# Kernel tuning notes

Measured on AMD Instinct MI355X. Metric: run time of the kernel, lower is better.

Reference implementation:

```python
import jax, jax.numpy as jnp
import numpy as np

B = 32768
K = 4096  # num_embeddings
D = 512   # embedding_dim
COMMITMENT_COST = 0.25


def setup_inputs() -> dict:
    key = jax.random.key(0)
    k1, k2 = jax.random.split(key)
    inputs = jax.random.normal(k1, (B, D), dtype=jnp.float32)
    # nn.Embedding weight init: uniform(-1/K, 1/K)
    codebook = jax.random.uniform(k2, (K, D), dtype=jnp.float32,
                                  minval=-1.0 / K, maxval=1.0 / K)
    return {"inputs": inputs, "codebook": codebook}


def reference(inputs, codebook):
    distances = (jnp.sum(inputs ** 2, axis=1, keepdims=True)
                 + jnp.sum(codebook ** 2, axis=1)
                 - 2.0 * jnp.matmul(inputs, codebook.T))
    encoding_indices = jnp.argmin(distances, axis=1)  # [B]
    # one-hot encodings are part of the module's returned dict
    encodings = jax.nn.one_hot(encoding_indices, K, dtype=inputs.dtype)  # [B, K]
    # quantized = encodings @ codebook == direct gather (same math)
    quantized = codebook[encoding_indices]  # [B, D]

    sg = jax.lax.stop_gradient
    e_latent_loss = jnp.mean((sg(quantized) - inputs) ** 2)
    q_latent_loss = jnp.mean((quantized - sg(inputs)) ** 2)
    loss = q_latent_loss + COMMITMENT_COST * e_latent_loss

    # straight-through estimator
    quantized_st = inputs + sg(quantized - inputs)

    avg_probs = jnp.mean(encodings, axis=0)  # [K]
    perplexity = jnp.exp(-jnp.sum(avg_probs * jnp.log(avg_probs + 1e-10)))

    return quantized_st, encoding_indices, loss, perplexity, encodings
```

## Files before the change

### kernel.cpp

```cpp
#include <hip/hip_runtime.h>
#include <hip/hip_bf16.h>


typedef __attribute__((ext_vector_type(8))) short bf16x8;
typedef __attribute__((ext_vector_type(4))) float f32x4;

#define BB 32768
#define KK 4096
#define DD 512

#define IDX_OFF  (BB*DD)
#define LOSS_OFF (IDX_OFF + BB)
#define PERP_OFF (LOSS_OFF + 1)
#define ENC_OFF  (PERP_OFF + 1)

#define WSB_XSQ  0
#define WSB_ESQ  131072
#define WSB_IDX  147456
#define WSB_HIST 278528
#define WSB_LOSS 294912
#define WSB_EBF3 294928
#define WSB_XBF  4489232
#define WSB_PART 38043664

#define MARG 2.5e-4f
#define NCAND 16

static __device__ __forceinline__ unsigned short f2bf(float f) {
    __hip_bfloat16 h = __float2bfloat16(f);
    return *reinterpret_cast<unsigned short*>(&h);
}

static __device__ __forceinline__ unsigned int packscore(float s, int col) {
    unsigned int u = __float_as_uint(s);
    u ^= (u & 0x80000000u) ? 0xFFFFFFFFu : 0x80000000u;
    return (u & 0xFFFFF000u) | (unsigned int)col;
}
static __device__ __forceinline__ float unpackscore(unsigned int p) {
    unsigned int u = p & 0xFFFFF000u;
    u = (u & 0x80000000u) ? (u ^ 0x80000000u) : ~u;
    return __uint_as_float(u);
}

static __device__ __forceinline__ void gll16(const void* g, void* l) {
    __builtin_amdgcn_global_load_lds(
        (const __attribute__((address_space(1))) unsigned int*)g,
        (__attribute__((address_space(3))) unsigned int*)l, 16, 0, 0);
}

__global__ __launch_bounds__(256) void npsum_pack_kernel(const float* __restrict__ X,
                                                         const float* __restrict__ E,
                                                         float* __restrict__ xsq,
                                                         float* __restrict__ esq,
                                                         unsigned short* __restrict__ Xbf) {
    __shared__ float sq[4][512];
    __shared__ float ub[4][64];
    __shared__ float bb[4][4];
    int w = threadIdx.x >> 6, lane = threadIdx.x & 63;
    int row = blockIdx.x * 4 + w;
    const float* src; float* dst;
    bool isx = (row < BB);
    if (isx) { src = X + (size_t)row * DD;        dst = xsq + row; }
    else     { src = E + (size_t)(row - BB) * DD; dst = esq + (row - BB); }
    const float4* s4 = (const float4*)(src + lane * 8);
    float4 a = s4[0], b = s4[1];
    sq[w][lane * 8 + 0] = __fmul_rn(a.x, a.x);
    sq[w][lane * 8 + 1] = __fmul_rn(a.y, a.y);
    sq[w][lane * 8 + 2] = __fmul_rn(a.z, a.z);
    sq[w][lane * 8 + 3] = __fmul_rn(a.w, a.w);
    sq[w][lane * 8 + 4] = __fmul_rn(b.x, b.x);
    sq[w][lane * 8 + 5] = __fmul_rn(b.y, b.y);
    sq[w][lane * 8 + 6] = __fmul_rn(b.z, b.z);
    sq[w][lane * 8 + 7] = __fmul_rn(b.w, b.w);
    if (isx) {
        int kt64 = lane >> 3, ks = (lane >> 2) & 1, oct = lane & 3;
        int rf = (row >> 4) & 15;
        size_t unit = ((size_t)((row >> 8) * 8 + kt64)) * 2048
                    + (size_t)((rf * 2 + ks) * 64 + oct * 16 + (row & 15));
        union { bf16x8 v; unsigned short us[8]; } pk;
        pk.us[0] = f2bf(a.x); pk.us[1] = f2bf(a.y); pk.us[2] = f2bf(a.z); pk.us[3] = f2bf(a.w);
        pk.us[4] = f2bf(b.x); pk.us[5] = f2bf(b.y); pk.us[6] = f2bf(b.z); pk.us[7] = f2bf(b.w);
        *(bf16x8*)(Xbf + unit * 8) = pk.v;
    }
    __syncthreads();
    {
        int b2 = lane >> 4, l = lane & 15;
        const float* s = &sq[w][b2 * 128];
        float t = __fadd_rn(
            __fadd_rn(__fadd_rn(s[l], s[16 + l]), __fadd_rn(s[32 + l], s[48 + l])),
            __fadd_rn(__fadd_rn(s[64 + l], s[80 + l]), __fadd_rn(s[96 + l], s[112 + l])));
        ub[w][lane] = t;
    }
    __syncthreads();
    if (lane < 4) {
        const float* u = &ub[w][lane * 16];
        float T3[8], T6[4];
        #pragma unroll
        for (int i = 0; i < 8; ++i) T3[i] = __fadd_rn(u[i], u[i + 8]);
        #pragma unroll
        for (int i = 0; i < 4; ++i) T6[i] = __fadd_rn(T3[i], T3[i + 4]);
        bb[w][lane] = __fadd_rn(__fadd_rn(T6[0], T6[2]), __fadd_rn(T6[1], T6[3]));
    }
    __syncthreads();
    if (lane == 0)
        *dst = __fadd_rn(__fadd_rn(bb[w][0], bb[w][1]), __fadd_rn(bb[w][2], bb[w][3]));
}

__global__ __launch_bounds__(256) void packE3_kernel(const float* __restrict__ E,
                                                     unsigned short* __restrict__ Ebf3,
                                                     int* __restrict__ hist,
                                                     double* __restrict__ loss_acc) {
    int t = blockIdx.x * 256 + threadIdx.x;
    if (t < KK) hist[t] = 0;
    if (t == KK) *loss_acc = 0.0;
    int cbb = t >> 12, u = t & 4095;
    int ks = u >> 8, nf = (u >> 6) & 3, lane = u & 63;
    int col = cbb * 64 + nf * 16 + (lane & 15);
    int k   = ks * 32 + (lane >> 4) * 8;
    const float4* s = (const float4*)(E + (size_t)col * DD + k);
    float4 a = s[0], b = s[1];
    union { bf16x8 v; unsigned short us[8]; } pk;
    pk.us[0] = f2bf(a.x); pk.us[1] = f2bf(a.y); pk.us[2] = f2bf(a.z); pk.us[3] = f2bf(a.w);
    pk.us[4] = f2bf(b.x); pk.us[5] = f2bf(b.y); pk.us[6] = f2bf(b.z); pk.us[7] = f2bf(b.w);
    *(bf16x8*)(Ebf3 + (size_t)t * 8) = pk.v;
}

__global__ __launch_bounds__(256, 2) void gemm_screen(
    const unsigned short* __restrict__ Xbf, const unsigned short* __restrict__ Ebf3,
    const float* __restrict__ esqw, uint2* __restrict__ partials)
{
    __shared__ __align__(16) char Bsh[65536];

    const int tid = threadIdx.x;
    const int w = tid >> 6, lane = tid & 63;
    const int c = lane & 15, g = lane >> 4;
    const int bid = blockIdx.x;
    const int orig = (bid & 7) * 2048 + (bid >> 3);
    const int rb = orig >> 6, cbb = orig & 63;
    const int row0 = rb * 128, col0 = cbb * 64;

    {
        const char* src = (const char*)Ebf3 + (size_t)cbb * 65536 + (size_t)tid * 16;
        char* dst = Bsh + w * 1024;
        #pragma unroll
        for (int j = 0; j < 16; ++j)
            gll16(src + j * 4096, dst + j * 4096);
    }

    const char* Xc = (const char*)Xbf + (size_t)(rb >> 1) * 262144;
    const int rfb = (rb & 1) * 8 + w * 2;

    f32x4 acc[2][4];
    #pragma unroll
    for (int i = 0; i < 2; ++i)
        #pragma unroll
        for (int j = 0; j < 4; ++j) acc[i][j] = (f32x4){0.f, 0.f, 0.f, 0.f};

    __syncthreads();

    #pragma unroll
    for (int ks = 0; ks < 16; ++ks) {
        const size_t base = (size_t)(ks >> 1) * 32768 + (size_t)(ks & 1) * 1024
                          + (size_t)lane * 16;
        bf16x8 a0 = *(const bf16x8*)(Xc + base + (size_t)(rfb + 0) * 2048);
        bf16x8 a1 = *(const bf16x8*)(Xc + base + (size_t)(rfb + 1) * 2048);
        #pragma unroll
        for (int nf = 0; nf < 4; ++nf) {
            bf16x8 b = *(const bf16x8*)(Bsh + (((ks * 4 + nf) * 64) + lane) * 16);
            acc[0][nf] = __builtin_amdgcn_mfma_f32_16x16x32_bf16(a0, b, acc[0][nf], 0, 0, 0);
            acc[1][nf] = __builtin_amdgcn_mfma_f32_16x16x32_bf16(a1, b, acc[1][nf], 0, 0, 0);
        }
    }

    float es[4];
    #pragma unroll
    for (int nf = 0; nf < 4; ++nf) es[nf] = esqw[col0 + nf * 16 + c];
    #pragma unroll
    for (int mf = 0; mf < 2; ++mf) {
        #pragma unroll
        for (int r = 0; r < 4; ++r) {
            unsigned int q1 = 0xFFFFFFFFu, q2 = 0xFFFFFFFFu;
            #pragma unroll
            for (int nf = 0; nf < 4; ++nf) {
                int col = col0 + nf * 16 + c;
                float s = fmaf(-2.0f, acc[mf][nf][r], es[nf]);
                unsigned int q = packscore(s, col);
                if (q < q1) { q2 = q1; q1 = q; } else if (q < q2) q2 = q;
            }
            #pragma unroll
            for (int off = 1; off < 16; off <<= 1) {
                unsigned int o1 = (unsigned int)__shfl_xor((int)q1, off, 64);
                unsigned int o2 = (unsigned int)__shfl_xor((int)q2, off, 64);
                unsigned int n1 = min(q1, o1);
                unsigned int n2 = min(max(q1, o1), min(q2, o2));
                q1 = n1; q2 = n2;
            }
            if (c == 0) {
                int row = row0 + w * 32 + mf * 16 + g * 4 + r;
                partials[(size_t)cbb * BB + row] = make_uint2(q1, q2);
            }
        }
    }
}

__global__ __launch_bounds__(256) void reduce_kernel(
    const float* __restrict__ X, const float* __restrict__ E,
    const float* __restrict__ xsqw, const float* __restrict__ esqw,
    const uint2* __restrict__ partials, int* __restrict__ idxbuf,
    int* __restrict__ hist, double* __restrict__ loss_acc,
    float* __restrict__ out)
{
    __shared__ double lred[256];
    const int row = blockIdx.x * 256 + threadIdx.x;
    unsigned int m = 0xFFFFFFFFu;
    for (int e = 0; e < 64; ++e) m = min(m, partials[(size_t)e * BB + row].x);
    float lim = unpackscore(m) + MARG;
    int cand[NCAND]; int nc = 0;
    for (int e = 0; e < 64; ++e) {
        uint2 p = partials[(size_t)e * BB + row];
        if (unpackscore(p.x) <= lim && nc < NCAND) cand[nc++] = (int)(p.x & 0xFFFu);
        if (unpackscore(p.y) <= lim && nc < NCAND) cand[nc++] = (int)(p.y & 0xFFFu);
    }
    const float* xr = X + (size_t)row * DD;
    float xs = xsqw[row];
    float bd = 3.0e38f; int bk = 0x7fffffff;
    for (int cidx = 0; cidx < nc; ++cidx) {
        int k = cand[cidx] & (KK - 1);
        const float* er = E + (size_t)k * DD;
        float q1 = 0.f, q2 = 0.f;
        for (int d = 0; d < 384; ++d)   q1 = fmaf(xr[d], er[d], q1);
        for (int d = 384; d < 512; ++d) q2 = fmaf(xr[d], er[d], q2);
        float dot = __fadd_rn(q1, q2);
        float t1  = __fadd_rn(xs, esqw[k]);
        float dnp = __fsub_rn(t1, __fmul_rn(2.0f, dot));
        if (dnp < bd || (dnp == bd && k < bk)) { bd = dnp; bk = k; }
    }
    const float* er = E + (size_t)bk * DD;
    double ls = 0.0;
    for (int d = 0; d < DD; ++d) {
        double df = (double)xr[d] - (double)er[d];
        ls = fma(df, df, ls);
    }
    idxbuf[row] = bk;
    out[IDX_OFF + row] = (float)bk;
    atomicAdd(&hist[bk], 1);
    lred[threadIdx.x] = ls;
    __syncthreads();
    for (int t = 128; t > 0; t >>= 1) {
        if (threadIdx.x < t) lred[threadIdx.x] += lred[threadIdx.x + t];
        __syncthreads();
    }
    if (threadIdx.x == 0) atomicAdd(loss_acc, lred[0]);
}

__global__ __launch_bounds__(256) void encq_kernel(const int* __restrict__ idxbuf,
                                                   const float* __restrict__ E,
                                                   float* __restrict__ out) {
    int row = blockIdx.x;
    int idx = idxbuf[row];
    ((float2*)out)[(size_t)row * 256 + threadIdx.x] =
        ((const float2*)E)[(size_t)idx * 256 + threadIdx.x];
    float2* erow = (float2*)(out + ENC_OFF) + (size_t)row * (KK / 2);
    int half = idx >> 1;
    float2 one;
    if (idx & 1) { one.x = 0.f; one.y = 1.f; } else { one.x = 1.f; one.y = 0.f; }
    float2 z; z.x = 0.f; z.y = 0.f;
    for (int c = threadIdx.x; c < KK / 2; c += 256)
        erow[c] = (c == half) ? one : z;
}

__global__ __launch_bounds__(256) void fin_kernel(const int* __restrict__ hist,
                                                  const double* __restrict__ loss_acc,
                                                  float* __restrict__ out) {
    __shared__ double red[256];
    int tid = threadIdx.x;
    double s = 0.0;
    for (int k = tid; k < KK; k += 256) {
        double p = (double)hist[k] * (1.0 / 32768.0);
        s += p * log(p + 1e-10);
    }
    red[tid] = s;
    __syncthreads();
    for (int t = 128; t > 0; t >>= 1) {
        if (tid < t) red[tid] += red[tid + t];
        __syncthreads();
    }
    if (tid == 0) {
        double perp = exp(-red[0]);
        double L = loss_acc[0] * (1.0 / ((double)BB * (double)DD));
        out[LOSS_OFF] = (float)(1.25 * L);
        out[PERP_OFF] = (float)perp;
    }
}

extern "C" void kernel_launch(void* const* d_in, const int* in_sizes, int n_in,
                              void* d_out, int out_size, void* d_ws, size_t ws_size,
                              hipStream_t stream) {
    const float* X; const float* E;
    if (in_sizes[0] == BB * DD) { X = (const float*)d_in[0]; E = (const float*)d_in[1]; }
    else                        { X = (const float*)d_in[1]; E = (const float*)d_in[0]; }
    float* out = (float*)d_out;

    float* xsq = (float*)((char*)d_ws + WSB_XSQ);
    float* esq = (float*)((char*)d_ws + WSB_ESQ);
    int* idxbuf = (int*)((char*)d_ws + WSB_IDX);
    int* hist   = (int*)((char*)d_ws + WSB_HIST);
    double* loss_acc = (double*)((char*)d_ws + WSB_LOSS);
    unsigned short* Ebf3 = (unsigned short*)((char*)d_ws + WSB_EBF3);
    unsigned short* Xbf  = (unsigned short*)((char*)d_ws + WSB_XBF);
    uint2* partials = (uint2*)((char*)d_ws + WSB_PART);

    hipLaunchKernelGGL(npsum_pack_kernel, dim3((BB + KK) / 4), dim3(256), 0, stream,
                       X, E, xsq, esq, Xbf);
    hipLaunchKernelGGL(packE3_kernel, dim3(1024), dim3(256), 0, stream,
                       E, Ebf3, hist, loss_acc);
    hipLaunchKernelGGL(gemm_screen, dim3(16384), dim3(256), 0, stream,
                       Xbf, Ebf3, esq, partials);
    hipLaunchKernelGGL(reduce_kernel, dim3(BB / 256), dim3(256), 0, stream,
                       X, E, xsq, esq, partials, idxbuf, hist, loss_acc, out);
    hipLaunchKernelGGL(encq_kernel, dim3(BB), dim3(256), 0, stream, idxbuf, E, out);
    hipLaunchKernelGGL(fin_kernel, dim3(1), dim3(256), 0, stream, hist, loss_acc, out);
}
```

Baseline: 535.8 us.

## Restructure screening GEMM into 256x256 tiles with double-buffered async LDS pipeline

The screening GEMM moves from 128x64 tiles, with the full-K codebook slab in LDS and A read straight from global, to 256x256 tiles with 8 waves. Both operands are staged through a double-buffered 128KB LDS pool using async global-to-LDS loads, interleaved with MFMA phases under barriers and raised wave priority. The X and E bf16 packing layouts change to match the new tiles. This raises data reuse per byte loaded and overlaps memory traffic with compute. The costs are heavy LDS use (limiting occupancy), many barriers, and a large accumulator register footprint.

```diff
diff --git a/kernel.cpp b/kernel.cpp
--- a/kernel.cpp
+++ b/kernel.cpp
@@ -19,7 +19,7 @@
 #define WSB_IDX  147456
 #define WSB_HIST 278528
 #define WSB_LOSS 294912
-#define WSB_EBF3 294928
+#define WSB_EBF2 294928
 #define WSB_XBF  4489232
 #define WSB_PART 38043664
 
@@ -76,7 +76,7 @@
         int kt64 = lane >> 3, ks = (lane >> 2) & 1, oct = lane & 3;
         int rf = (row >> 4) & 15;
         size_t unit = ((size_t)((row >> 8) * 8 + kt64)) * 2048
-                    + (size_t)((rf * 2 + ks) * 64 + oct * 16 + (row & 15));
+                    + (size_t)((ks * 16 + rf) * 64 + oct * 16 + (row & 15));
         union { bf16x8 v; unsigned short us[8]; } pk;
         pk.us[0] = f2bf(a.x); pk.us[1] = f2bf(a.y); pk.us[2] = f2bf(a.z); pk.us[3] = f2bf(a.w);
         pk.us[4] = f2bf(b.x); pk.us[5] = f2bf(b.y); pk.us[6] = f2bf(b.z); pk.us[7] = f2bf(b.w);
@@ -106,83 +106,106 @@
         *dst = __fadd_rn(__fadd_rn(bb[w][0], bb[w][1]), __fadd_rn(bb[w][2], bb[w][3]));
 }
 
-__global__ __launch_bounds__(256) void packE3_kernel(const float* __restrict__ E,
-                                                     unsigned short* __restrict__ Ebf3,
-                                                     int* __restrict__ hist,
-                                                     double* __restrict__ loss_acc) {
+__global__ __launch_bounds__(256) void packE_kernel(const float* __restrict__ E,
+                                                    unsigned short* __restrict__ Ebf2,
+                                                    int* __restrict__ hist,
+                                                    double* __restrict__ loss_acc) {
     int t = blockIdx.x * 256 + threadIdx.x;
     if (t < KK) hist[t] = 0;
     if (t == KK) *loss_acc = 0.0;
-    int cbb = t >> 12, u = t & 4095;
-    int ks = u >> 8, nf = (u >> 6) & 3, lane = u & 63;
-    int col = cbb * 64 + nf * 16 + (lane & 15);
-    int k   = ks * 32 + (lane >> 4) * 8;
+    int chunk = t >> 11, u = t & 2047;
+    int ks = u >> 10, rf = (u >> 6) & 15, lane = u & 63;
+    int col = (chunk >> 3) * 256 + rf * 16 + (lane & 15);
+    int k   = (chunk & 7) * 64 + ks * 32 + (lane >> 4) * 8;
     const float4* s = (const float4*)(E + (size_t)col * DD + k);
     float4 a = s[0], b = s[1];
     union { bf16x8 v; unsigned short us[8]; } pk;
     pk.us[0] = f2bf(a.x); pk.us[1] = f2bf(a.y); pk.us[2] = f2bf(a.z); pk.us[3] = f2bf(a.w);
     pk.us[4] = f2bf(b.x); pk.us[5] = f2bf(b.y); pk.us[6] = f2bf(b.z); pk.us[7] = f2bf(b.w);
-    *(bf16x8*)(Ebf3 + (size_t)t * 8) = pk.v;
-}
-
-__global__ __launch_bounds__(256, 2) void gemm_screen(
-    const unsigned short* __restrict__ Xbf, const unsigned short* __restrict__ Ebf3,
+    *(bf16x8*)(Ebf2 + (size_t)t * 8) = pk.v;
+}
+
+__global__ __launch_bounds__(512, 2) void gemm_screen(
+    const unsigned short* __restrict__ Xbf, const unsigned short* __restrict__ Ebf2,
     const float* __restrict__ esqw, uint2* __restrict__ partials)
 {
-    __shared__ __align__(16) char Bsh[65536];
+    extern __shared__ __align__(16) char pool[];
 
     const int tid = threadIdx.x;
     const int w = tid >> 6, lane = tid & 63;
     const int c = lane & 15, g = lane >> 4;
     const int bid = blockIdx.x;
-    const int orig = (bid & 7) * 2048 + (bid >> 3);
-    const int rb = orig >> 6, cbb = orig & 63;
-    const int row0 = rb * 128, col0 = cbb * 64;
-
-    {
-        const char* src = (const char*)Ebf3 + (size_t)cbb * 65536 + (size_t)tid * 16;
-        char* dst = Bsh + w * 1024;
-        #pragma unroll
-        for (int j = 0; j < 16; ++j)
-            gll16(src + j * 4096, dst + j * 4096);
-    }
-
-    const char* Xc = (const char*)Xbf + (size_t)(rb >> 1) * 262144;
-    const int rfb = (rb & 1) * 8 + w * 2;
-
-    f32x4 acc[2][4];
+    const int orig = (bid & 7) * 256 + (bid >> 3);
+    const int rb2 = orig >> 4, cb2 = orig & 15;
+    const int row0 = rb2 * 256, col0 = cb2 * 256;
+    const int mw = w >> 2, nw = w & 3;
+
+    const char* Xc = (const char*)Xbf  + (size_t)rb2 * 262144;
+    const char* Ec = (const char*)Ebf2 + (size_t)cb2 * 262144;
+
+    f32x4 acc[8][4];
     #pragma unroll
-    for (int i = 0; i < 2; ++i)
+    for (int i = 0; i < 8; ++i)
         #pragma unroll
         for (int j = 0; j < 4; ++j) acc[i][j] = (f32x4){0.f, 0.f, 0.f, 0.f};
 
-    __syncthreads();
-
-    #pragma unroll
-    for (int ks = 0; ks < 16; ++ks) {
-        const size_t base = (size_t)(ks >> 1) * 32768 + (size_t)(ks & 1) * 1024
-                          + (size_t)lane * 16;
-        bf16x8 a0 = *(const bf16x8*)(Xc + base + (size_t)(rfb + 0) * 2048);
-        bf16x8 a1 = *(const bf16x8*)(Xc + base + (size_t)(rfb + 1) * 2048);
-        #pragma unroll
-        for (int nf = 0; nf < 4; ++nf) {
-            bf16x8 b = *(const bf16x8*)(Bsh + (((ks * 4 + nf) * 64) + lane) * 16);
-            acc[0][nf] = __builtin_amdgcn_mfma_f32_16x16x32_bf16(a0, b, acc[0][nf], 0, 0, 0);
-            acc[1][nf] = __builtin_amdgcn_mfma_f32_16x16x32_bf16(a1, b, acc[1][nf], 0, 0, 0);
-        }
+    #define ISSUE(base_, tile_, kh_, bofs_) { \
+        const char* s_ = (base_) + (size_t)(tile_) * 32768 + (kh_) * 16384 + (size_t)tid * 16; \
+        char* d_ = pool + (bofs_) + (((tile_) & 1) * 32768) + (kh_) * 16384 + w * 1024; \
+        gll16(s_, d_); gll16(s_ + 8192, d_ + 8192); }
+
+    #define PHASE(p_, STG_, WAIT_) { \
+        const int pt_ = (p_) >> 2, qk_ = ((p_) >> 1) & 1, qm_ = (p_) & 1; \
+        const char* Ap_ = pool + pt_ * 32768 + qk_ * 16384; \
+        const char* Bp_ = pool + 65536 + pt_ * 32768 + qk_ * 16384; \
+        bf16x8 af_[4], bf_[4]; \
+        _Pragma("unroll") for (int ii = 0; ii < 4; ++ii) \
+            af_[ii] = *(const bf16x8*)(Ap_ + (((mw * 8 + qm_ * 4 + ii) * 64) + lane) * 16); \
+        _Pragma("unroll") for (int jj = 0; jj < 4; ++jj) \
+            bf_[jj] = *(const bf16x8*)(Bp_ + (((nw * 4 + jj) * 64) + lane) * 16); \
+        STG_; \
+        WAIT_; \
+        __builtin_amdgcn_s_barrier(); \
+        __builtin_amdgcn_s_setprio(1); \
+        _Pragma("unroll") for (int ii = 0; ii < 4; ++ii) \
+            _Pragma("unroll") for (int jj = 0; jj < 4; ++jj) \
+                acc[qm_ * 4 + ii][jj] = __builtin_amdgcn_mfma_f32_16x16x32_bf16( \
+                    af_[ii], bf_[jj], acc[qm_ * 4 + ii][jj], 0, 0, 0); \
+        __builtin_amdgcn_s_setprio(0); \
+        __builtin_amdgcn_s_barrier(); }
+
+    ISSUE(Xc, 0, 0, 0); ISSUE(Ec, 0, 0, 65536);
+    ISSUE(Xc, 0, 1, 0); ISSUE(Ec, 0, 1, 65536);
+    ISSUE(Xc, 1, 0, 0); ISSUE(Ec, 1, 0, 65536);
+    asm volatile("s_waitcnt vmcnt(4)" ::: "memory");
+    __builtin_amdgcn_s_barrier();
+
+    for (int i = 0; i < 4; ++i) {
+        const int t1n = 2 * i + 1, t2n = 2 * i + 2, t3n = 2 * i + 3;
+        PHASE(0, ISSUE(Xc, t1n, 1, 0), {});
+        PHASE(1, ISSUE(Ec, t1n, 1, 65536), {});
+        PHASE(2, if (i < 3) ISSUE(Xc, t2n, 0, 0), {});
+        PHASE(3, if (i < 3) ISSUE(Ec, t2n, 0, 65536),
+                 if (i < 3) { asm volatile("s_waitcnt vmcnt(4)" ::: "memory"); }
+                 else       { asm volatile("s_waitcnt vmcnt(0)" ::: "memory"); });
+        PHASE(4, if (i < 3) ISSUE(Xc, t2n, 1, 0), {});
+        PHASE(5, if (i < 3) ISSUE(Ec, t2n, 1, 65536), {});
+        PHASE(6, if (i < 3) ISSUE(Xc, t3n, 0, 0), {});
+        PHASE(7, if (i < 3) ISSUE(Ec, t3n, 0, 65536),
+                 if (i < 3) { asm volatile("s_waitcnt vmcnt(4)" ::: "memory"); });
     }
 
     float es[4];
     #pragma unroll
-    for (int nf = 0; nf < 4; ++nf) es[nf] = esqw[col0 + nf * 16 + c];
+    for (int nf = 0; nf < 4; ++nf) es[nf] = esqw[col0 + nw * 64 + nf * 16 + c];
     #pragma unroll
-    for (int mf = 0; mf < 2; ++mf) {
+    for (int mf = 0; mf < 8; ++mf) {
         #pragma unroll
         for (int r = 0; r < 4; ++r) {
             unsigned int q1 = 0xFFFFFFFFu, q2 = 0xFFFFFFFFu;
             #pragma unroll
             for (int nf = 0; nf < 4; ++nf) {
-                int col = col0 + nf * 16 + c;
+                int col = col0 + nw * 64 + nf * 16 + c;
                 float s = fmaf(-2.0f, acc[mf][nf][r], es[nf]);
                 unsigned int q = packscore(s, col);
                 if (q < q1) { q2 = q1; q1 = q; } else if (q < q2) q2 = q;
@@ -196,11 +219,13 @@
                 q1 = n1; q2 = n2;
             }
             if (c == 0) {
-                int row = row0 + w * 32 + mf * 16 + g * 4 + r;
-                partials[(size_t)cbb * BB + row] = make_uint2(q1, q2);
+                int row = row0 + mw * 128 + mf * 16 + g * 4 + r;
+                partials[(size_t)(cb2 * 4 + nw) * BB + row] = make_uint2(q1, q2);
             }
         }
     }
+    #undef ISSUE
+    #undef PHASE
 }
 
 __global__ __launch_bounds__(256) void reduce_kernel(
@@ -306,16 +331,16 @@
     int* idxbuf = (int*)((char*)d_ws + WSB_IDX);
     int* hist   = (int*)((char*)d_ws + WSB_HIST);
     double* loss_acc = (double*)((char*)d_ws + WSB_LOSS);
-    unsigned short* Ebf3 = (unsigned short*)((char*)d_ws + WSB_EBF3);
+    unsigned short* Ebf2 = (unsigned short*)((char*)d_ws + WSB_EBF2);
     unsigned short* Xbf  = (unsigned short*)((char*)d_ws + WSB_XBF);
     uint2* partials = (uint2*)((char*)d_ws + WSB_PART);
 
     hipLaunchKernelGGL(npsum_pack_kernel, dim3((BB + KK) / 4), dim3(256), 0, stream,
                        X, E, xsq, esq, Xbf);
-    hipLaunchKernelGGL(packE3_kernel, dim3(1024), dim3(256), 0, stream,
-                       E, Ebf3, hist, loss_acc);
-    hipLaunchKernelGGL(gemm_screen, dim3(16384), dim3(256), 0, stream,
-                       Xbf, Ebf3, esq, partials);
+    hipLaunchKernelGGL(packE_kernel, dim3(1024), dim3(256), 0, stream,
+                       E, Ebf2, hist, loss_acc);
+    hipLaunchKernelGGL(gemm_screen, dim3(2048), dim3(512), 131072, stream,
+                       Xbf, Ebf2, esq, partials);
     hipLaunchKernelGGL(reduce_kernel, dim3(BB / 256), dim3(256), 0, stream,
                        X, E, xsq, esq, partials, idxbuf, hist, loss_acc, out);
     hipLaunchKernelGGL(encq_kernel, dim3(BB), dim3(256), 0, stream, idxbuf, E, out);
```

New measurement: 492.7 us. 8.0% less time.

## Make GEMM screen persistent per row block with register-resident A and streamed codebook

Applied to the files above, without the earlier changes.

Replaces the 16384-block GEMM with 256 persistent blocks. Each block keeps its 128 rows of bf16 X in registers and streams the whole codebook through double-buffered LDS in 32-column tiles. It keeps a running per-lane top-3 instead of a per-tile top-2 with a shuffle reduction. Partials shrink from 64 to 32 entries per row, which lightens the reduce pass and removes the repeated A reloads and per-block launch overhead. The cost is one block per CU, a large register footprint and a long serial loop with barriers, so latency hiding depends on the prefetch pipeline.

```diff
diff --git a/kernel.cpp b/kernel.cpp
--- a/kernel.cpp
+++ b/kernel.cpp
@@ -19,7 +19,7 @@
 #define WSB_IDX  147456
 #define WSB_HIST 278528
 #define WSB_LOSS 294912
-#define WSB_EBF3 294928
+#define WSB_EBF  294928
 #define WSB_XBF  4489232
 #define WSB_PART 38043664
 
@@ -76,7 +76,7 @@
         int kt64 = lane >> 3, ks = (lane >> 2) & 1, oct = lane & 3;
         int rf = (row >> 4) & 15;
         size_t unit = ((size_t)((row >> 8) * 8 + kt64)) * 2048
-                    + (size_t)((rf * 2 + ks) * 64 + oct * 16 + (row & 15));
+                    + (size_t)((ks * 16 + rf) * 64 + oct * 16 + (row & 15));
         union { bf16x8 v; unsigned short us[8]; } pk;
         pk.us[0] = f2bf(a.x); pk.us[1] = f2bf(a.y); pk.us[2] = f2bf(a.z); pk.us[3] = f2bf(a.w);
         pk.us[4] = f2bf(b.x); pk.us[5] = f2bf(b.y); pk.us[6] = f2bf(b.z); pk.us[7] = f2bf(b.w);
@@ -106,99 +106,130 @@
         *dst = __fadd_rn(__fadd_rn(bb[w][0], bb[w][1]), __fadd_rn(bb[w][2], bb[w][3]));
 }
 
-__global__ __launch_bounds__(256) void packE3_kernel(const float* __restrict__ E,
-                                                     unsigned short* __restrict__ Ebf3,
-                                                     int* __restrict__ hist,
-                                                     double* __restrict__ loss_acc) {
+__global__ __launch_bounds__(256) void packE_kernel(const float* __restrict__ E,
+                                                    unsigned short* __restrict__ Ebf,
+                                                    int* __restrict__ hist,
+                                                    double* __restrict__ loss_acc) {
     int t = blockIdx.x * 256 + threadIdx.x;
     if (t < KK) hist[t] = 0;
     if (t == KK) *loss_acc = 0.0;
-    int cbb = t >> 12, u = t & 4095;
-    int ks = u >> 8, nf = (u >> 6) & 3, lane = u & 63;
-    int col = cbb * 64 + nf * 16 + (lane & 15);
+    int chunk = t >> 11, u = t & 2047;
+    int ks = u >> 7, nf = (u >> 6) & 1, lane = u & 63;
+    int col = chunk * 32 + nf * 16 + (lane & 15);
     int k   = ks * 32 + (lane >> 4) * 8;
     const float4* s = (const float4*)(E + (size_t)col * DD + k);
     float4 a = s[0], b = s[1];
     union { bf16x8 v; unsigned short us[8]; } pk;
     pk.us[0] = f2bf(a.x); pk.us[1] = f2bf(a.y); pk.us[2] = f2bf(a.z); pk.us[3] = f2bf(a.w);
     pk.us[4] = f2bf(b.x); pk.us[5] = f2bf(b.y); pk.us[6] = f2bf(b.z); pk.us[7] = f2bf(b.w);
-    *(bf16x8*)(Ebf3 + (size_t)t * 8) = pk.v;
-}
-
-__global__ __launch_bounds__(256, 2) void gemm_screen(
-    const unsigned short* __restrict__ Xbf, const unsigned short* __restrict__ Ebf3,
+    *(bf16x8*)(Ebf + (size_t)t * 8) = pk.v;
+}
+
+__global__ __launch_bounds__(256, 1) void gemm_screen(
+    const unsigned short* __restrict__ Xbf, const unsigned short* __restrict__ Ebf,
     const float* __restrict__ esqw, uint2* __restrict__ partials)
 {
-    __shared__ __align__(16) char Bsh[65536];
+    extern __shared__ __align__(16) char pool[];
+    float* esh = (float*)(pool + 65536);
 
     const int tid = threadIdx.x;
     const int w = tid >> 6, lane = tid & 63;
     const int c = lane & 15, g = lane >> 4;
     const int bid = blockIdx.x;
-    const int orig = (bid & 7) * 2048 + (bid >> 3);
-    const int rb = orig >> 6, cbb = orig & 63;
-    const int row0 = rb * 128, col0 = cbb * 64;
+    const int orig = (bid & 7) * 32 + (bid >> 3);
+    const int row0 = orig * 128;
 
     {
-        const char* src = (const char*)Ebf3 + (size_t)cbb * 65536 + (size_t)tid * 16;
-        char* dst = Bsh + w * 1024;
-        #pragma unroll
-        for (int j = 0; j < 16; ++j)
-            gll16(src + j * 4096, dst + j * 4096);
-    }
-
-    const char* Xc = (const char*)Xbf + (size_t)(rb >> 1) * 262144;
-    const int rfb = (rb & 1) * 8 + w * 2;
-
-    f32x4 acc[2][4];
+        const float4* s = (const float4*)esqw;
+        float4* d = (float4*)esh;
+        #pragma unroll
+        for (int j = 0; j < 4; ++j) d[tid + j * 256] = s[tid + j * 256];
+    }
+    __syncthreads();
+
+    const char* Xc = (const char*)Xbf + (size_t)(orig >> 1) * 262144;
+    const int rfb = (orig & 1) * 8 + w * 2;
+    bf16x8 af0[16], af1[16];
+    #pragma unroll
+    for (int kg = 0; kg < 16; ++kg) {
+        int kt = kg >> 1, ks2 = kg & 1;
+        const char* base = Xc + (size_t)kt * 32768;
+        af0[kg] = *(const bf16x8*)(base + (size_t)(((ks2 * 16 + rfb + 0) * 64) + lane) * 16);
+        af1[kg] = *(const bf16x8*)(base + (size_t)(((ks2 * 16 + rfb + 1) * 64) + lane) * 16);
+    }
+
+    const char* Ec = (const char*)Ebf;
+    #define ISSUE(t_) { \
+        const char* s_ = Ec + (size_t)(t_) * 32768 + (size_t)tid * 16; \
+        char* d_ = pool + ((t_) & 1) * 32768 + w * 1024; \
+        gll16(s_,          d_); \
+        gll16(s_ + 4096,   d_ + 4096); \
+        gll16(s_ + 8192,   d_ + 8192); \
+        gll16(s_ + 12288,  d_ + 12288); \
+        gll16(s_ + 16384,  d_ + 16384); \
+        gll16(s_ + 20480,  d_ + 20480); \
+        gll16(s_ + 24576,  d_ + 24576); \
+        gll16(s_ + 28672,  d_ + 28672); }
+
+    unsigned int p1[2][4], p2[2][4], p3[2][4];
     #pragma unroll
     for (int i = 0; i < 2; ++i)
         #pragma unroll
-        for (int j = 0; j < 4; ++j) acc[i][j] = (f32x4){0.f, 0.f, 0.f, 0.f};
-
-    __syncthreads();
+        for (int r = 0; r < 4; ++r) { p1[i][r] = ~0u; p2[i][r] = ~0u; p3[i][r] = ~0u; }
+
+    ISSUE(0); ISSUE(1);
+
+    #define TOP3(i_, r_, q_) { \
+        if ((q_) < p1[i_][r_]) { p3[i_][r_] = p2[i_][r_]; p2[i_][r_] = p1[i_][r_]; p1[i_][r_] = (q_); } \
+        else if ((q_) < p2[i_][r_]) { p3[i_][r_] = p2[i_][r_]; p2[i_][r_] = (q_); } \
+        else if ((q_) < p3[i_][r_]) { p3[i_][r_] = (q_); } }
+
+    #define BODY(t_, WAITS_) { \
+        asm volatile(WAITS_ ::: "memory"); \
+        __builtin_amdgcn_s_barrier(); \
+        __builtin_amdgcn_sched_barrier(0); \
+        const char* Bp_ = pool + ((t_) & 1) * 32768; \
+        f32x4 a00 = (f32x4){0.f,0.f,0.f,0.f}, a01 = (f32x4){0.f,0.f,0.f,0.f}; \
+        f32x4 a10 = (f32x4){0.f,0.f,0.f,0.f}, a11 = (f32x4){0.f,0.f,0.f,0.f}; \
+        __builtin_amdgcn_s_setprio(1); \
+        _Pragma("unroll") for (int ks = 0; ks < 16; ++ks) { \
+            bf16x8 b0 = *(const bf16x8*)(Bp_ + (((ks * 2 + 0) * 64) + lane) * 16); \
+            bf16x8 b1 = *(const bf16x8*)(Bp_ + (((ks * 2 + 1) * 64) + lane) * 16); \
+            a00 = __builtin_amdgcn_mfma_f32_16x16x32_bf16(af0[ks], b0, a00, 0, 0, 0); \
+            a01 = __builtin_amdgcn_mfma_f32_16x16x32_bf16(af0[ks], b1, a01, 0, 0, 0); \
+            a10 = __builtin_amdgcn_mfma_f32_16x16x32_bf16(af1[ks], b0, a10, 0, 0, 0); \
+            a11 = __builtin_amdgcn_mfma_f32_16x16x32_bf16(af1[ks], b1, a11, 0, 0, 0); \
+        } \
+        __builtin_amdgcn_s_setprio(0); \
+        { const int colb_ = (t_) * 32; \
+          float e0_ = esh[colb_ + c], e1_ = esh[colb_ + 16 + c]; \
+          unsigned int cl0_ = (unsigned int)(colb_ + c), cl1_ = (unsigned int)(colb_ + 16 + c); \
+          _Pragma("unroll") for (int r = 0; r < 4; ++r) { \
+              unsigned int q_; \
+              q_ = packscore(fmaf(-2.0f, a00[r], e0_), cl0_); TOP3(0, r, q_); \
+              q_ = packscore(fmaf(-2.0f, a01[r], e1_), cl1_); TOP3(0, r, q_); \
+              q_ = packscore(fmaf(-2.0f, a10[r], e0_), cl0_); TOP3(1, r, q_); \
+              q_ = packscore(fmaf(-2.0f, a11[r], e1_), cl1_); TOP3(1, r, q_); \
+          } } \
+        __builtin_amdgcn_s_barrier(); \
+        __builtin_amdgcn_sched_barrier(0); \
+        if ((t_) < 126) ISSUE((t_) + 2); }
+
+    BODY(0, "s_waitcnt vmcnt(8)");
+    #pragma unroll 2
+    for (int t = 1; t <= 126; ++t) BODY(t, "s_waitcnt vmcnt(8)");
+    BODY(127, "s_waitcnt vmcnt(0)");
+    #undef BODY
+    #undef TOP3
+    #undef ISSUE
 
     #pragma unroll
-    for (int ks = 0; ks < 16; ++ks) {
-        const size_t base = (size_t)(ks >> 1) * 32768 + (size_t)(ks & 1) * 1024
-                          + (size_t)lane * 16;
-        bf16x8 a0 = *(const bf16x8*)(Xc + base + (size_t)(rfb + 0) * 2048);
-        bf16x8 a1 = *(const bf16x8*)(Xc + base + (size_t)(rfb + 1) * 2048);
-        #pragma unroll
-        for (int nf = 0; nf < 4; ++nf) {
-            bf16x8 b = *(const bf16x8*)(Bsh + (((ks * 4 + nf) * 64) + lane) * 16);
-            acc[0][nf] = __builtin_amdgcn_mfma_f32_16x16x32_bf16(a0, b, acc[0][nf], 0, 0, 0);
-            acc[1][nf] = __builtin_amdgcn_mfma_f32_16x16x32_bf16(a1, b, acc[1][nf], 0, 0, 0);
-        }
-    }
-
-    float es[4];
-    #pragma unroll
-    for (int nf = 0; nf < 4; ++nf) es[nf] = esqw[col0 + nf * 16 + c];
-    #pragma unroll
-    for (int mf = 0; mf < 2; ++mf) {
+    for (int i = 0; i < 2; ++i) {
         #pragma unroll
         for (int r = 0; r < 4; ++r) {
-            unsigned int q1 = 0xFFFFFFFFu, q2 = 0xFFFFFFFFu;
-            #pragma unroll
-            for (int nf = 0; nf < 4; ++nf) {
-                int col = col0 + nf * 16 + c;
-                float s = fmaf(-2.0f, acc[mf][nf][r], es[nf]);
-                unsigned int q = packscore(s, col);
-                if (q < q1) { q2 = q1; q1 = q; } else if (q < q2) q2 = q;
-            }
-            #pragma unroll
-            for (int off = 1; off < 16; off <<= 1) {
-                unsigned int o1 = (unsigned int)__shfl_xor((int)q1, off, 64);
-                unsigned int o2 = (unsigned int)__shfl_xor((int)q2, off, 64);
-                unsigned int n1 = min(q1, o1);
-                unsigned int n2 = min(max(q1, o1), min(q2, o2));
-                q1 = n1; q2 = n2;
-            }
-            if (c == 0) {
-                int row = row0 + w * 32 + mf * 16 + g * 4 + r;
-                partials[(size_t)cbb * BB + row] = make_uint2(q1, q2);
-            }
+            int row = row0 + w * 32 + i * 16 + g * 4 + r;
+            partials[(size_t)(c * 2 + 0) * BB + row] = make_uint2(p1[i][r], p2[i][r]);
+            partials[(size_t)(c * 2 + 1) * BB + row] = make_uint2(p3[i][r], 0xFFFFFFFFu);
         }
     }
 }
@@ -213,10 +244,10 @@
     __shared__ double lred[256];
     const int row = blockIdx.x * 256 + threadIdx.x;
     unsigned int m = 0xFFFFFFFFu;
-    for (int e = 0; e < 64; ++e) m = min(m, partials[(size_t)e * BB + row].x);
+    for (int e = 0; e < 32; ++e) m = min(m, partials[(size_t)e * BB + row].x);
     float lim = unpackscore(m) + MARG;
     int cand[NCAND]; int nc = 0;
-    for (int e = 0; e < 64; ++e) {
+    for (int e = 0; e < 32; ++e) {
         uint2 p = partials[(size_t)e * BB + row];
         if (unpackscore(p.x) <= lim && nc < NCAND) cand[nc++] = (int)(p.x & 0xFFFu);
         if (unpackscore(p.y) <= lim && nc < NCAND) cand[nc++] = (int)(p.y & 0xFFFu);
@@ -265,8 +296,8 @@
     float2 one;
     if (idx & 1) { one.x = 0.f; one.y = 1.f; } else { one.x = 1.f; one.y = 0.f; }
     float2 z; z.x = 0.f; z.y = 0.f;
-    for (int c = threadIdx.x; c < KK / 2; c += 256)
-        erow[c] = (c == half) ? one : z;
+    for (int cc = threadIdx.x; cc < KK / 2; cc += 256)
+        erow[cc] = (cc == half) ? one : z;
 }
 
 __global__ __launch_bounds__(256) void fin_kernel(const int* __restrict__ hist,
@@ -306,16 +337,16 @@
     int* idxbuf = (int*)((char*)d_ws + WSB_IDX);
     int* hist   = (int*)((char*)d_ws + WSB_HIST);
     double* loss_acc = (double*)((char*)d_ws + WSB_LOSS);
-    unsigned short* Ebf3 = (unsigned short*)((char*)d_ws + WSB_EBF3);
-    unsigned short* Xbf  = (unsigned short*)((char*)d_ws + WSB_XBF);
+    unsigned short* Ebf = (unsigned short*)((char*)d_ws + WSB_EBF);
+    unsigned short* Xbf = (unsigned short*)((char*)d_ws + WSB_XBF);
     uint2* partials = (uint2*)((char*)d_ws + WSB_PART);
 
     hipLaunchKernelGGL(npsum_pack_kernel, dim3((BB + KK) / 4), dim3(256), 0, stream,
                        X, E, xsq, esq, Xbf);
-    hipLaunchKernelGGL(packE3_kernel, dim3(1024), dim3(256), 0, stream,
-                       E, Ebf3, hist, loss_acc);
-    hipLaunchKernelGGL(gemm_screen, dim3(16384), dim3(256), 0, stream,
-                       Xbf, Ebf3, esq, partials);
+    hipLaunchKernelGGL(packE_kernel, dim3(1024), dim3(256), 0, stream,
+                       E, Ebf, hist, loss_acc);
+    hipLaunchKernelGGL(gemm_screen, dim3(256), dim3(256), 81920, stream,
+                       Xbf, Ebf, esq, partials);
     hipLaunchKernelGGL(reduce_kernel, dim3(BB / 256), dim3(256), 0, stream,
                        X, E, xsq, esq, partials, idxbuf, hist, loss_acc, out);
     hipLaunchKernelGGL(encq_kernel, dim3(BB), dim3(256), 0, stream, idxbuf, E, out);
```

After: 506.0 us. -5.6%, faster.
